# Kernel tuning notes

Hardware: AMD Instinct MI355X
Metric: run time of the kernel (lower is better)

Reference implementation:

```python
import jax, jax.numpy as jnp
import numpy as np

# Architecture constants (match init_kwargs)
L, M, K, P, G = 3, 4096, 2, 4, 4
NUM_IN, NUM_OUT, B = 8192, 1000, 2048
F = 6          # number of combinact activation functions
EPS_BN = 1e-5  # BatchNorm1d eps
EPS = 1e-12    # numeric safety for sqrt


def setup_inputs() -> dict:
    key = jax.random.key(0)
    ks = jax.random.split(key, 8)
    x = jax.random.normal(ks[0], (B, NUM_IN), jnp.float32)
    # shuffle maps: perm 0 is identity (the un-permuted copy), perms 1..P-1 random
    rng = np.random.default_rng(0)
    perms = np.stack([
        np.stack([np.arange(M)] + [rng.permutation(M) for _ in range(P - 1)])
        for _ in range(L)
    ]).astype(np.int32)  # (L, P, M)
    cin_g = NUM_IN // G  # per-group input width (curr stays 8192 every layer)
    W = jax.random.normal(ks[1], (L, G, M // G, cin_g), jnp.float32) / np.sqrt(cin_g)
    b = jax.random.normal(ks[2], (L, G, M // G), jnp.float32) * 0.01
    gamma = jnp.ones((L, M), jnp.float32)
    beta = jnp.zeros((L, M), jnp.float32)
    # original inits alpha_primes to zeros; small random gives non-degenerate mixing
    alpha = jax.random.normal(ks[3], (L, P, F), jnp.float32) * 0.1
    d_last = (M // K) * P
    W_out = jax.random.normal(ks[4], (NUM_OUT, d_last), jnp.float32) / np.sqrt(d_last)
    b_out = jnp.zeros((NUM_OUT,), jnp.float32)
    return {"x": x, "perms": jnp.asarray(perms), "W": W, "b": b,
            "gamma": gamma, "beta": beta, "alpha": alpha,
            "W_out": W_out, "b_out": b_out}


def _combinact(z, alpha_l):
    # z: (B, clusters, K, P) -> (B, clusters, P); per-perm softmax mixing
    sig = jax.nn.sigmoid(z)
    pr = jnp.prod(z, axis=2)
    acts = jnp.stack([
        jnp.max(z, axis=2),                          # max
        jnp.sign(pr) * jnp.sqrt(jnp.abs(pr) + EPS),  # signed geomean (k=2)
        z[:, :, 0, :] * jnp.prod(sig, axis=2),       # swish-k
        jnp.sqrt(jnp.sum(z * z, axis=2) + EPS),      # l2
        jnp.max(jnp.abs(z), axis=2),                 # linf
        jax.nn.logsumexp(z, axis=2),                 # lse
    ], axis=0)  # (F, B, clusters, P)
    w = jax.nn.softmax(alpha_l, axis=-1)  # (P, F)
    return jnp.einsum('fbcp,pf->bcp', acts, w)


def _forward(x, perms, W, b, gamma, beta, alpha, W_out, b_out):
    h = x
    for l in range(L):
        C = h.shape[1]
        # grouped small linears: (B, C/G, G) x (G, M/G, C/G) -> (B, M/G, G) -> (B, M)
        hr = h.reshape(B, C // G, G)
        y = jnp.einsum('bcg,gmc->bmg', hr, W[l]) + b[l].T[None]
        y = y.reshape(B, M)
        # BatchNorm1d (training mode, biased batch var)
        mu = jnp.mean(y, axis=0)
        var = jnp.mean((y - mu) ** 2, axis=0)
        y = (y - mu) * jax.lax.rsqrt(var + EPS_BN) * gamma[l] + beta[l]
        # p permuted copies, reshape into clusters of k
        zc = y[:, perms[l]]                                   # (B, P, M) gather
        z = jnp.transpose(zc, (0, 2, 1)).reshape(B, M // K, K, P)
        a = _combinact(z, alpha[l])                           # (B, M/K, P)
        h = jnp.transpose(a, (0, 2, 1)).reshape(B, (M // K) * P)
    return h @ W_out.T + b_out


def reference(x, perms, W, b, gamma, beta, alpha, W_out, b_out):
    return _forward(x, perms, W, b, gamma, beta, alpha, W_out, b_out)
```

## Files before the change

kernel.cpp:

```cpp
#include <hip/hip_runtime.h>
#include <math.h>

#define Lnum 3
#define Mdim 4096
#define Pdim 4
#define Gdim 4
#define NIN 8192
#define NOUT 1000
#define Bdim 2048
#define Fdim 6
#define CIN 2048
#define MG 1024
#define CH 2048
#define DNEXT 8192
#define NRCHUNK (Bdim / 128)

typedef short bf16x8 __attribute__((ext_vector_type(8)));
typedef float f32x4 __attribute__((ext_vector_type(4)));

__device__ __forceinline__ short f2bf(float f) {
    union { float f; unsigned u; } v; v.f = f;
    unsigned u = v.u;
    unsigned r = (u + 0x7fffu + ((u >> 16) & 1u)) >> 16;
    return (short)r;
}
__device__ __forceinline__ float bf2f(short h) {
    union { unsigned u; float f; } x;
    x.u = ((unsigned)(unsigned short)h) << 16;
    return x.f;
}

__global__ __launch_bounds__(256) void convert_f32_bf16(
    const float* __restrict__ src, short* __restrict__ dst, int n8)
{
    int i = blockIdx.x * 256 + threadIdx.x;
    if (i >= n8) return;
    const float4* s = (const float4*)src + (size_t)i * 2;
    float4 v0 = s[0], v1 = s[1];
    bf16x8 o;
    o[0] = f2bf(v0.x); o[1] = f2bf(v0.y); o[2] = f2bf(v0.z); o[3] = f2bf(v0.w);
    o[4] = f2bf(v1.x); o[5] = f2bf(v1.y); o[6] = f2bf(v1.z); o[7] = f2bf(v1.w);
    *((bf16x8*)dst + i) = o;
}

__global__ __launch_bounds__(256) void convert_wo(
    const float* __restrict__ src, short* __restrict__ dst)
{
    int i = blockIdx.x * 256 + threadIdx.x;
    int row = i >> 10;
    bf16x8 o;
    if (row < NOUT) {
        const float4* s = (const float4*)(src + (size_t)row * DNEXT + (i & 1023) * 8);
        float4 v0 = s[0], v1 = s[1];
        o[0] = f2bf(v0.x); o[1] = f2bf(v0.y); o[2] = f2bf(v0.z); o[3] = f2bf(v0.w);
        o[4] = f2bf(v1.x); o[5] = f2bf(v1.y); o[6] = f2bf(v1.z); o[7] = f2bf(v1.w);
    } else {
        for (int j = 0; j < 8; ++j) o[j] = 0;
    }
    *((bf16x8*)dst + i) = o;
}

__global__ __launch_bounds__(256) void x_to_grouped(
    const float* __restrict__ x, short* __restrict__ hg)
{
    const int c = blockIdx.x * 256 + threadIdx.x;
    const int b = blockIdx.y;
    float4 v = *(const float4*)(x + (size_t)b * NIN + 4 * c);
    const size_t plane = (size_t)Bdim * CIN;
    hg[0 * plane + (size_t)b * CIN + c] = f2bf(v.x);
    hg[1 * plane + (size_t)b * CIN + c] = f2bf(v.y);
    hg[2 * plane + (size_t)b * CIN + c] = f2bf(v.z);
    hg[3 * plane + (size_t)b * CIN + c] = f2bf(v.w);
}

__global__ __launch_bounds__(256) void remap_perms(
    const int* __restrict__ perm, int* __restrict__ perm_g, int n)
{
    int i = blockIdx.x * 256 + threadIdx.x;
    if (i >= n) return;
    int j  = perm[i];
    int jg = ((j & 3) << 10) | (j >> 2);
    perm_g[i] = jg ^ ((jg >> 3) & 3);
}

template<int BN_T, int NWARP, bool STATS, typename CT>
__global__ __launch_bounds__(NWARP * 64) void gemm_mfma(
    const short* __restrict__ A0, size_t aZ, int lda,
    const short* __restrict__ B0, size_t bZ, int ldb,
    const float* __restrict__ bias0, size_t biasZ,
    CT* __restrict__ C0, size_t cZ,
    int K, int ldc, int nbound,
    float* __restrict__ psum, float* __restrict__ psumsq, int sgz)
{
    constexpr int NT   = NWARP * 64;
    constexpr int WCN  = NWARP / 2;
    constexpr int WCOL = BN_T / WCN;
    constexpr int FN   = WCOL / 16;

    const int nx = gridDim.x, ny = gridDim.y;
    const int nwg = nx * ny * gridDim.z;
    const int lin = blockIdx.x + nx * (blockIdx.y + ny * blockIdx.z);
    int swz = (lin & 7) * (nwg >> 3) + (lin >> 3);
    const int bx = swz % nx; swz /= nx;
    const int by = swz % ny;
    const int g  = swz / ny;

    const short* A  = A0 + aZ * g;
    const short* Bm = B0 + bZ * g;
    CT* C = C0 + cZ * g;

    const int n0 = bx * BN_T;
    const int b0 = by * 128;

    __shared__ short As[2][128 * 64];
    __shared__ short Bs[2][BN_T * 64];

    const int tid  = threadIdx.x;
    const int w    = tid >> 6;
    const int lane = tid & 63;
    const int wr = w / WCN, wc = w % WCN;

    f32x4 acc[4][FN];
#pragma unroll
    for (int m = 0; m < 4; ++m)
#pragma unroll
        for (int n = 0; n < FN; ++n) acc[m][n] = (f32x4)0.f;

    auto stage = [&](int buf, int k0) {
#pragma unroll
        for (int idx = tid; idx < 128 * 8; idx += NT) {
            const int r = idx >> 3, slot = idx & 7;
            const int gs = slot ^ (r & 7);
            const short* ga = A + (size_t)(b0 + r) * lda + k0 + gs * 8;
            __builtin_amdgcn_global_load_lds(
                (const __attribute__((address_space(1))) void*)ga,
                (__attribute__((address_space(3))) void*)(&As[buf][idx * 8]), 16, 0, 0);
        }
#pragma unroll
        for (int idx = tid; idx < BN_T * 8; idx += NT) {
            const int r = idx >> 3, slot = idx & 7;
            const int gs = slot ^ (r & 7);
            const short* gb = Bm + (size_t)(n0 + r) * ldb + k0 + gs * 8;
            __builtin_amdgcn_global_load_lds(
                (const __attribute__((address_space(1))) void*)gb,
                (__attribute__((address_space(3))) void*)(&Bs[buf][idx * 8]), 16, 0, 0);
        }
    };

    const int fr15 = lane & 15;
    const int fq   = lane >> 4;

    auto compute = [&](int buf) {
#pragma unroll
        for (int kk = 0; kk < 2; ++kk) {
            bf16x8 af[4], bff[FN];
            const int kob = kk * 64 + fq * 16;
#pragma unroll
            for (int m = 0; m < 4; ++m) {
                const int r  = wr * 64 + m * 16 + fr15;
                const int sw = kob ^ ((r & 7) << 4);
                af[m] = *(const bf16x8*)(&As[buf][r * 64 + (sw >> 1)]);
            }
#pragma unroll
            for (int n = 0; n < FN; ++n) {
                const int r  = wc * WCOL + n * 16 + fr15;
                const int sw = kob ^ ((r & 7) << 4);
                bff[n] = *(const bf16x8*)(&Bs[buf][r * 64 + (sw >> 1)]);
            }
#pragma unroll
            for (int m = 0; m < 4; ++m)
#pragma unroll
                for (int n = 0; n < FN; ++n)
                    acc[m][n] = __builtin_amdgcn_mfma_f32_16x16x32_bf16(af[m], bff[n], acc[m][n], 0, 0, 0);
        }
    };

    stage(0, 0);

    const int nt = K >> 6;
    int p = 0;
    for (int t = 0; t < nt - 1; ++t) {
        stage(p ^ 1, (t + 1) << 6);
        asm volatile("s_waitcnt vmcnt(4)" ::: "memory");
        __builtin_amdgcn_s_barrier();
        asm volatile("" ::: "memory");
        compute(p);
        asm volatile("" ::: "memory");
        __builtin_amdgcn_s_barrier();
        p ^= 1;
    }
    asm volatile("s_waitcnt vmcnt(0)" ::: "memory");
    __builtin_amdgcn_s_barrier();
    asm volatile("" ::: "memory");
    compute(p);

    float s[FN], ss[FN];
#pragma unroll
    for (int n = 0; n < FN; ++n) { s[n] = 0.f; ss[n] = 0.f; }

#pragma unroll
    for (int m = 0; m < 4; ++m) {
#pragma unroll
        for (int n = 0; n < FN; ++n) {
#pragma unroll
            for (int j = 0; j < 4; ++j) {
                const int row = b0 + wr * 64 + m * 16 + fq * 4 + j;
                const int col = n0 + wc * WCOL + n * 16 + fr15;
                if (col < nbound) {
                    float v = acc[m][n][j];
                    if (bias0) v += bias0[biasZ * g + col];
                    C[(size_t)row * ldc + col] = (CT)(sizeof(CT) == 2 ? (CT)f2bf(v) : (CT)v);
                    if (STATS) { s[n] += v; ss[n] += v * v; }
                }
            }
        }
    }

    if (STATS) {
        __syncthreads();
        float* sum_lds = (float*)&As[0][0];
        float* ssq_lds = sum_lds + BN_T * 8;
        const int slot = wr * 4 + fq;
#pragma unroll
        for (int n = 0; n < FN; ++n) {
            const int cl = wc * WCOL + n * 16 + fr15;
            sum_lds[cl * 8 + slot] = s[n];
            ssq_lds[cl * 8 + slot] = ss[n];
        }
        __syncthreads();
        for (int cl = tid; cl < BN_T; cl += NT) {
            float a = 0.f, b = 0.f;
#pragma unroll
            for (int q = 0; q < 8; ++q) {
                a += sum_lds[cl * 8 + q];
                b += ssq_lds[cl * 8 + q];
            }
            const size_t o = (size_t)by * Mdim + g * sgz + n0 + cl;
            psum[o]   = a;
            psumsq[o] = b;
        }
    }
}

__global__ __launch_bounds__(256) void reduce_out(
    const float* __restrict__ part, const float* __restrict__ bo,
    float* __restrict__ out)
{
    const int n = blockIdx.x * 256 + threadIdx.x;
    const int b = blockIdx.y;
    if (n >= NOUT) return;
    const size_t S = (size_t)Bdim * 1024;
    const size_t i = (size_t)b * 1024 + n;
    out[(size_t)b * NOUT + n] =
        part[i] + part[S + i] + part[2 * S + i] + part[3 * S + i] + bo[n];
}

__global__ __launch_bounds__(256) void bn_finalize(
    const float* __restrict__ psum, const float* __restrict__ psumsq,
    const float* __restrict__ gamma, const float* __restrict__ beta,
    float* __restrict__ scale, float* __restrict__ shift)
{
    const int jg = blockIdx.x * 256 + threadIdx.x;
    if (jg >= Mdim) return;
    const int j = ((jg & 1023) << 2) | (jg >> 10);
    float s = 0.f, ss = 0.f;
    for (int r = 0; r < NRCHUNK; ++r) {
        s  += psum[r * Mdim + jg];
        ss += psumsq[r * Mdim + jg];
    }
    const float mu  = s * (1.f / Bdim);
    const float var = ss * (1.f / Bdim) - mu * mu;
    const float sc  = gamma[j] * rsqrtf(var + 1e-5f);
    scale[jg] = sc;
    shift[jg] = beta[j] - mu * sc;
}

__global__ void alpha_softmax(const float* __restrict__ alpha, float* __restrict__ wsm)
{
    const int idx = threadIdx.x;
    if (idx >= Lnum * Pdim) return;
    const float* a = alpha + idx * Fdim;
    float mx = a[0];
#pragma unroll
    for (int f = 1; f < Fdim; ++f) mx = fmaxf(mx, a[f]);
    float e[Fdim]; float s = 0.f;
#pragma unroll
    for (int f = 0; f < Fdim; ++f) { e[f] = __expf(a[f] - mx); s += e[f]; }
    const float inv = 1.f / s;
#pragma unroll
    for (int f = 0; f < Fdim; ++f) wsm[idx * Fdim + f] = e[f] * inv;
}

template<int MODE>
__global__ __launch_bounds__(256) void combinact_kernel(
    const short* __restrict__ Y, const float* __restrict__ scale,
    const float* __restrict__ shift, const int* __restrict__ perm,
    const float* __restrict__ wsm, short* __restrict__ out)
{
    __shared__ f32x4 yn4[Mdim];
    const int b0  = blockIdx.x * 4;
    const int tid = threadIdx.x;

#pragma unroll
    for (int k = 0; k < 2; ++k) {
        const int i8   = k * 256 + tid;
        const int base = i8 * 8;
        const bf16x8 v0 = *((const bf16x8*)(Y + (size_t)(b0 + 0) * Mdim) + i8);
        const bf16x8 v1 = *((const bf16x8*)(Y + (size_t)(b0 + 1) * Mdim) + i8);
        const bf16x8 v2 = *((const bf16x8*)(Y + (size_t)(b0 + 2) * Mdim) + i8);
        const bf16x8 v3 = *((const bf16x8*)(Y + (size_t)(b0 + 3) * Mdim) + i8);
        const int xr = i8 & 3;
#pragma unroll
        for (int jj = 0; jj < 8; ++jj) {
            const float sc = scale[base + jj];
            const float sh = shift[base + jj];
            f32x4 t;
            t[0] = bf2f(v0[jj]) * sc + sh;
            t[1] = bf2f(v1[jj]) * sc + sh;
            t[2] = bf2f(v2[jj]) * sc + sh;
            t[3] = bf2f(v3[jj]) * sc + sh;
            yn4[base + (jj ^ xr)] = t;
        }
    }
    __syncthreads();

    float wv[Pdim][Fdim];
#pragma unroll
    for (int p = 0; p < Pdim; ++p)
#pragma unroll
        for (int f = 0; f < Fdim; ++f) wv[p][f] = wsm[p * Fdim + f];

    const float L2E = 1.44269504f;
    const float LN2 = 0.69314718f;
    const size_t plane = (size_t)Bdim * CIN;

#pragma unroll
    for (int k = 0; k < 8; ++k) {
        const int idx = k * 256 + tid;
        int c, g = 0, q = 0;
        if (MODE == 0) { g = idx >> 9; q = idx & 511; c = q * 4 + g; }
        else           { c = idx; }

#pragma unroll
        for (int p = 0; p < Pdim; ++p) {
            const int2 jj = *(const int2*)(perm + p * Mdim + 2 * c);
            const f32x4 z0v = yn4[jj.x];
            const f32x4 z1v = yn4[jj.y];

#pragma unroll
            for (int r = 0; r < 4; ++r) {
                const float z0 = z0v[r];
                const float z1 = z1v[r];

                const float mx = fmaxf(z0, z1);
                const float pr = z0 * z1;
                const float a1 = copysignf(__builtin_amdgcn_sqrtf(fabsf(pr) + 1e-12f), pr);

                const float e0 = __builtin_amdgcn_exp2f(-L2E * z0);
                const float e1 = __builtin_amdgcn_exp2f(-L2E * z1);
                const float a2 = z0 * __builtin_amdgcn_rcpf((1.f + e0) * (1.f + e1));

                const float a3 = __builtin_amdgcn_sqrtf(z0 * z0 + z1 * z1 + 1e-12f);
                const float a4 = fmaxf(fabsf(z0), fabsf(z1));

                const float ed = __builtin_amdgcn_exp2f(-L2E * fabsf(z0 - z1));
                const float a5 = mx + LN2 * __builtin_amdgcn_logf(1.f + ed);

                const float v = wv[p][0] * mx + wv[p][1] * a1 + wv[p][2] * a2 +
                                wv[p][3] * a3 + wv[p][4] * a4 + wv[p][5] * a5;

                if (MODE == 0)
                    out[g * plane + (size_t)(b0 + r) * CIN + p * 512 + q] = f2bf(v);
                else
                    out[(size_t)(b0 + r) * DNEXT + p * CH + c] = f2bf(v);
            }
        }
    }
}

extern "C" void kernel_launch(void* const* d_in, const int* in_sizes, int n_in,
                              void* d_out, int out_size, void* d_ws, size_t ws_size,
                              hipStream_t stream)
{
    const float* x     = (const float*)d_in[0];
    const int*   perms = (const int*)  d_in[1];
    const float* W     = (const float*)d_in[2];
    const float* bvec  = (const float*)d_in[3];
    const float* gamma = (const float*)d_in[4];
    const float* beta  = (const float*)d_in[5];
    const float* alpha = (const float*)d_in[6];
    const float* Wo    = (const float*)d_in[7];
    const float* bo    = (const float*)d_in[8];
    float* out = (float*)d_out;

    char* ws = (char*)d_ws;
    short* y      = (short*)ws;
    short* hg     = y + (size_t)Bdim * Mdim;
    short* Wlb3   = hg + (size_t)Gdim * Bdim * CIN;
    short* Wob    = Wlb3 + (size_t)Lnum * Gdim * MG * CIN;
    float* psum   = (float*)(Wob + (size_t)1024 * DNEXT);
    float* psumsq = psum + (size_t)NRCHUNK * Mdim;
    float* scale  = psumsq + (size_t)NRCHUNK * Mdim;
    float* shift  = scale + Mdim;
    float* wsm    = shift + Mdim;
    int*   perm_g = (int*)(wsm + Lnum * Pdim * Fdim);

    short* hflat = hg;
    float* part  = (float*)Wlb3;

    alpha_softmax<<<1, 64, 0, stream>>>(alpha, wsm);
    remap_perms<<<(Lnum * Pdim * Mdim) / 256, 256, 0, stream>>>(
        perms, perm_g, Lnum * Pdim * Mdim);
    convert_f32_bf16<<<(Lnum * Gdim * MG * CIN / 8) / 256, 256, 0, stream>>>(
        W, Wlb3, Lnum * Gdim * MG * CIN / 8);
    convert_wo<<<(1024 * 1024) / 256, 256, 0, stream>>>(Wo, Wob);
    x_to_grouped<<<dim3(CIN / 256, Bdim), 256, 0, stream>>>(x, hg);

    const size_t planeA = (size_t)Bdim * CIN;
    const size_t planeB = (size_t)MG * CIN;

    for (int l = 0; l < Lnum; ++l) {
        dim3 gg(MG / 128, Bdim / 128, Gdim);
        gemm_mfma<128, 8, true, short><<<gg, 512, 0, stream>>>(
            hg, planeA, CIN, Wlb3 + (size_t)l * Gdim * MG * CIN, planeB, CIN,
            bvec + (size_t)l * Gdim * MG, (size_t)MG,
            y, (size_t)MG,
            CIN, Mdim, MG,
            psum, psumsq, MG);

        bn_finalize<<<Mdim / 256, 256, 0, stream>>>(
            psum, psumsq, gamma + (size_t)l * Mdim, beta + (size_t)l * Mdim, scale, shift);

        if (l < Lnum - 1)
            combinact_kernel<0><<<Bdim / 4, 256, 0, stream>>>(
                y, scale, shift, perm_g + (size_t)l * Pdim * Mdim, wsm + l * Pdim * Fdim, hg);
        else
            combinact_kernel<1><<<Bdim / 4, 256, 0, stream>>>(
                y, scale, shift, perm_g + (size_t)l * Pdim * Mdim, wsm + l * Pdim * Fdim, hflat);
    }

    dim3 go(1024 / 128, Bdim / 128, 4);
    gemm_mfma<128, 8, false, float><<<go, 512, 0, stream>>>(
        hflat, (size_t)2048, DNEXT, Wob, (size_t)2048, DNEXT,
        nullptr, 0,
        part, (size_t)Bdim * 1024,
        2048, 1024, 1024,
        nullptr, nullptr, 0);

    dim3 gr(4, Bdim);
    reduce_out<<<gr, 256, 0, stream>>>(part, bo, out);
}
```

Before: 316.2 us.

## Fuse weight fp32-to-bf16 conversion into GEMM B staging and precompute exps in combinact

Removes the separate weight conversion kernels. The GEMMs now read fp32 weights directly, convert them in registers and write the swizzled bf16 into LDS, with the pipeline restructured so the global loads overlap compute. The combinact kernel now handles 2 batch rows per block and stores exp(z) alongside z in shared memory. It then derives swish, and logsumexp as log(E0+E1), from the stored exps instead of recomputing three exps per pair. The GEMMs read twice the weight bytes and convert them repeatedly across tiles, and log(E0+E1) can overflow for large z.

```diff
diff --git a/kernel.cpp b/kernel.cpp
--- a/kernel.cpp
+++ b/kernel.cpp
@@ -1,4 +1,5 @@
 #include <hip/hip_runtime.h>
+#include <hip/hip_bf16.h>
 #include <math.h>
 
 #define Lnum 3
@@ -30,36 +31,6 @@
     return x.f;
 }
 
-__global__ __launch_bounds__(256) void convert_f32_bf16(
-    const float* __restrict__ src, short* __restrict__ dst, int n8)
-{
-    int i = blockIdx.x * 256 + threadIdx.x;
-    if (i >= n8) return;
-    const float4* s = (const float4*)src + (size_t)i * 2;
-    float4 v0 = s[0], v1 = s[1];
-    bf16x8 o;
-    o[0] = f2bf(v0.x); o[1] = f2bf(v0.y); o[2] = f2bf(v0.z); o[3] = f2bf(v0.w);
-    o[4] = f2bf(v1.x); o[5] = f2bf(v1.y); o[6] = f2bf(v1.z); o[7] = f2bf(v1.w);
-    *((bf16x8*)dst + i) = o;
-}
-
-__global__ __launch_bounds__(256) void convert_wo(
-    const float* __restrict__ src, short* __restrict__ dst)
-{
-    int i = blockIdx.x * 256 + threadIdx.x;
-    int row = i >> 10;
-    bf16x8 o;
-    if (row < NOUT) {
-        const float4* s = (const float4*)(src + (size_t)row * DNEXT + (i & 1023) * 8);
-        float4 v0 = s[0], v1 = s[1];
-        o[0] = f2bf(v0.x); o[1] = f2bf(v0.y); o[2] = f2bf(v0.z); o[3] = f2bf(v0.w);
-        o[4] = f2bf(v1.x); o[5] = f2bf(v1.y); o[6] = f2bf(v1.z); o[7] = f2bf(v1.w);
-    } else {
-        for (int j = 0; j < 8; ++j) o[j] = 0;
-    }
-    *((bf16x8*)dst + i) = o;
-}
-
 __global__ __launch_bounds__(256) void x_to_grouped(
     const float* __restrict__ x, short* __restrict__ hg)
 {
@@ -86,7 +57,7 @@
 template<int BN_T, int NWARP, bool STATS, typename CT>
 __global__ __launch_bounds__(NWARP * 64) void gemm_mfma(
     const short* __restrict__ A0, size_t aZ, int lda,
-    const short* __restrict__ B0, size_t bZ, int ldb,
+    const float* __restrict__ B0, size_t bZ, int ldb, int bclamp,
     const float* __restrict__ bias0, size_t biasZ,
     CT* __restrict__ C0, size_t cZ,
     int K, int ldc, int nbound,
@@ -106,7 +77,7 @@
     const int g  = swz / ny;
 
     const short* A  = A0 + aZ * g;
-    const short* Bm = B0 + bZ * g;
+    const float* Bf = B0 + bZ * g;
     CT* C = C0 + cZ * g;
 
     const int n0 = bx * BN_T;
@@ -126,7 +97,7 @@
 #pragma unroll
         for (int n = 0; n < FN; ++n) acc[m][n] = (f32x4)0.f;
 
-    auto stage = [&](int buf, int k0) {
+    auto stageA = [&](int buf, int k0) {
 #pragma unroll
         for (int idx = tid; idx < 128 * 8; idx += NT) {
             const int r = idx >> 3, slot = idx & 7;
@@ -136,15 +107,30 @@
                 (const __attribute__((address_space(1))) void*)ga,
                 (__attribute__((address_space(3))) void*)(&As[buf][idx * 8]), 16, 0, 0);
         }
-#pragma unroll
-        for (int idx = tid; idx < BN_T * 8; idx += NT) {
-            const int r = idx >> 3, slot = idx & 7;
-            const int gs = slot ^ (r & 7);
-            const short* gb = Bm + (size_t)(n0 + r) * ldb + k0 + gs * 8;
-            __builtin_amdgcn_global_load_lds(
-                (const __attribute__((address_space(1))) void*)gb,
-                (__attribute__((address_space(3))) void*)(&Bs[buf][idx * 8]), 16, 0, 0);
-        }
+    };
+
+    static_assert(NT == BN_T * 4, "B-staging mapping assumes 4 threads/row");
+    const int brow = tid >> 2;
+    const int bq   = tid & 3;
+    float4 br0, br1, br2, br3;
+    auto issueB = [&](int k0) {
+        const int rr = min(n0 + brow, bclamp - 1);
+        const float* p = Bf + (size_t)rr * ldb + k0 + bq * 16;
+        br0 = *(const float4*)(p);
+        br1 = *(const float4*)(p + 4);
+        br2 = *(const float4*)(p + 8);
+        br3 = *(const float4*)(p + 12);
+    };
+    auto writeB = [&](int buf) {
+        bf16x8 o0, o1;
+        o0[0] = f2bf(br0.x); o0[1] = f2bf(br0.y); o0[2] = f2bf(br0.z); o0[3] = f2bf(br0.w);
+        o0[4] = f2bf(br1.x); o0[5] = f2bf(br1.y); o0[6] = f2bf(br1.z); o0[7] = f2bf(br1.w);
+        o1[0] = f2bf(br2.x); o1[1] = f2bf(br2.y); o1[2] = f2bf(br2.z); o1[3] = f2bf(br2.w);
+        o1[4] = f2bf(br3.x); o1[5] = f2bf(br3.y); o1[6] = f2bf(br3.z); o1[7] = f2bf(br3.w);
+        const int s0 = (2 * bq)     ^ (brow & 7);
+        const int s1 = (2 * bq + 1) ^ (brow & 7);
+        *(bf16x8*)(&Bs[buf][brow * 64 + s0 * 8]) = o0;
+        *(bf16x8*)(&Bs[buf][brow * 64 + s1 * 8]) = o1;
     };
 
     const int fr15 = lane & 15;
@@ -175,24 +161,28 @@
         }
     };
 
-    stage(0, 0);
+    stageA(0, 0);
+    issueB(0);
+    asm volatile("s_waitcnt vmcnt(0)" ::: "memory");
+    writeB(0);
+    asm volatile("s_waitcnt lgkmcnt(0)" ::: "memory");
+    __builtin_amdgcn_s_barrier();
+    asm volatile("" ::: "memory");
 
     const int nt = K >> 6;
     int p = 0;
-    for (int t = 0; t < nt - 1; ++t) {
-        stage(p ^ 1, (t + 1) << 6);
-        asm volatile("s_waitcnt vmcnt(4)" ::: "memory");
+    for (int t = 0; t < nt; ++t) {
+        if (t + 1 < nt) { stageA(p ^ 1, (t + 1) << 6); issueB((t + 1) << 6); }
+        compute(p);
+        if (t + 1 < nt) {
+            asm volatile("s_waitcnt vmcnt(0)" ::: "memory");
+            writeB(p ^ 1);
+        }
+        asm volatile("s_waitcnt lgkmcnt(0)" ::: "memory");
         __builtin_amdgcn_s_barrier();
         asm volatile("" ::: "memory");
-        compute(p);
-        asm volatile("" ::: "memory");
-        __builtin_amdgcn_s_barrier();
         p ^= 1;
     }
-    asm volatile("s_waitcnt vmcnt(0)" ::: "memory");
-    __builtin_amdgcn_s_barrier();
-    asm volatile("" ::: "memory");
-    compute(p);
 
     float s[FN], ss[FN];
 #pragma unroll
@@ -297,9 +287,11 @@
     const float* __restrict__ shift, const int* __restrict__ perm,
     const float* __restrict__ wsm, short* __restrict__ out)
 {
-    __shared__ f32x4 yn4[Mdim];
-    const int b0  = blockIdx.x * 4;
+    __shared__ f32x4 zE[Mdim];
+    const int b0  = blockIdx.x * 2;
     const int tid = threadIdx.x;
+    const float L2E = 1.44269504f;
+    const float LN2 = 0.69314718f;
 
 #pragma unroll
     for (int k = 0; k < 2; ++k) {
@@ -307,8 +299,6 @@
         const int base = i8 * 8;
         const bf16x8 v0 = *((const bf16x8*)(Y + (size_t)(b0 + 0) * Mdim) + i8);
         const bf16x8 v1 = *((const bf16x8*)(Y + (size_t)(b0 + 1) * Mdim) + i8);
-        const bf16x8 v2 = *((const bf16x8*)(Y + (size_t)(b0 + 2) * Mdim) + i8);
-        const bf16x8 v3 = *((const bf16x8*)(Y + (size_t)(b0 + 3) * Mdim) + i8);
         const int xr = i8 & 3;
 #pragma unroll
         for (int jj = 0; jj < 8; ++jj) {
@@ -317,9 +307,9 @@
             f32x4 t;
             t[0] = bf2f(v0[jj]) * sc + sh;
             t[1] = bf2f(v1[jj]) * sc + sh;
-            t[2] = bf2f(v2[jj]) * sc + sh;
-            t[3] = bf2f(v3[jj]) * sc + sh;
-            yn4[base + (jj ^ xr)] = t;
+            t[2] = __builtin_amdgcn_exp2f(L2E * t[0]);
+            t[3] = __builtin_amdgcn_exp2f(L2E * t[1]);
+            zE[base + (jj ^ xr)] = t;
         }
     }
     __syncthreads();
@@ -330,8 +320,6 @@
 #pragma unroll
         for (int f = 0; f < Fdim; ++f) wv[p][f] = wsm[p * Fdim + f];
 
-    const float L2E = 1.44269504f;
-    const float LN2 = 0.69314718f;
     const size_t plane = (size_t)Bdim * CIN;
 
 #pragma unroll
@@ -344,27 +332,22 @@
 #pragma unroll
         for (int p = 0; p < Pdim; ++p) {
             const int2 jj = *(const int2*)(perm + p * Mdim + 2 * c);
-            const f32x4 z0v = yn4[jj.x];
-            const f32x4 z1v = yn4[jj.y];
-
-#pragma unroll
-            for (int r = 0; r < 4; ++r) {
-                const float z0 = z0v[r];
-                const float z1 = z1v[r];
+            const f32x4 c0 = zE[jj.x];
+            const f32x4 c1 = zE[jj.y];
+
+#pragma unroll
+            for (int r = 0; r < 2; ++r) {
+                const float z0 = c0[r],     z1 = c1[r];
+                const float E0 = c0[2 + r], E1 = c1[2 + r];
 
                 const float mx = fmaxf(z0, z1);
                 const float pr = z0 * z1;
                 const float a1 = copysignf(__builtin_amdgcn_sqrtf(fabsf(pr) + 1e-12f), pr);
-
-                const float e0 = __builtin_amdgcn_exp2f(-L2E * z0);
-                const float e1 = __builtin_amdgcn_exp2f(-L2E * z1);
-                const float a2 = z0 * __builtin_amdgcn_rcpf((1.f + e0) * (1.f + e1));
-
+                const float a2 = z0 * E0 * E1 *
+                                 __builtin_amdgcn_rcpf((1.f + E0) * (1.f + E1));
                 const float a3 = __builtin_amdgcn_sqrtf(z0 * z0 + z1 * z1 + 1e-12f);
                 const float a4 = fmaxf(fabsf(z0), fabsf(z1));
-
-                const float ed = __builtin_amdgcn_exp2f(-L2E * fabsf(z0 - z1));
-                const float a5 = mx + LN2 * __builtin_amdgcn_logf(1.f + ed);
+                const float a5 = LN2 * __builtin_amdgcn_logf(E0 + E1);
 
                 const float v = wv[p][0] * mx + wv[p][1] * a1 + wv[p][2] * a2 +
                                 wv[p][3] * a3 + wv[p][4] * a4 + wv[p][5] * a5;
@@ -396,9 +379,8 @@
     char* ws = (char*)d_ws;
     short* y      = (short*)ws;
     short* hg     = y + (size_t)Bdim * Mdim;
-    short* Wlb3   = hg + (size_t)Gdim * Bdim * CIN;
-    short* Wob    = Wlb3 + (size_t)Lnum * Gdim * MG * CIN;
-    float* psum   = (float*)(Wob + (size_t)1024 * DNEXT);
+    float* part   = (float*)(hg + (size_t)Gdim * Bdim * CIN);
+    float* psum   = part + (size_t)4 * Bdim * 1024;
     float* psumsq = psum + (size_t)NRCHUNK * Mdim;
     float* scale  = psumsq + (size_t)NRCHUNK * Mdim;
     float* shift  = scale + Mdim;
@@ -406,14 +388,10 @@
     int*   perm_g = (int*)(wsm + Lnum * Pdim * Fdim);
 
     short* hflat = hg;
-    float* part  = (float*)Wlb3;
 
     alpha_softmax<<<1, 64, 0, stream>>>(alpha, wsm);
     remap_perms<<<(Lnum * Pdim * Mdim) / 256, 256, 0, stream>>>(
         perms, perm_g, Lnum * Pdim * Mdim);
-    convert_f32_bf16<<<(Lnum * Gdim * MG * CIN / 8) / 256, 256, 0, stream>>>(
-        W, Wlb3, Lnum * Gdim * MG * CIN / 8);
-    convert_wo<<<(1024 * 1024) / 256, 256, 0, stream>>>(Wo, Wob);
     x_to_grouped<<<dim3(CIN / 256, Bdim), 256, 0, stream>>>(x, hg);
 
     const size_t planeA = (size_t)Bdim * CIN;
@@ -422,7 +400,8 @@
     for (int l = 0; l < Lnum; ++l) {
         dim3 gg(MG / 128, Bdim / 128, Gdim);
         gemm_mfma<128, 8, true, short><<<gg, 512, 0, stream>>>(
-            hg, planeA, CIN, Wlb3 + (size_t)l * Gdim * MG * CIN, planeB, CIN,
+            hg, planeA, CIN,
+            W + (size_t)l * Gdim * MG * CIN, planeB, CIN, MG,
             bvec + (size_t)l * Gdim * MG, (size_t)MG,
             y, (size_t)MG,
             CIN, Mdim, MG,
@@ -432,16 +411,17 @@
             psum, psumsq, gamma + (size_t)l * Mdim, beta + (size_t)l * Mdim, scale, shift);
 
         if (l < Lnum - 1)
-            combinact_kernel<0><<<Bdim / 4, 256, 0, stream>>>(
+            combinact_kernel<0><<<Bdim / 2, 256, 0, stream>>>(
                 y, scale, shift, perm_g + (size_t)l * Pdim * Mdim, wsm + l * Pdim * Fdim, hg);
         else
-            combinact_kernel<1><<<Bdim / 4, 256, 0, stream>>>(
+            combinact_kernel<1><<<Bdim / 2, 256, 0, stream>>>(
                 y, scale, shift, perm_g + (size_t)l * Pdim * Mdim, wsm + l * Pdim * Fdim, hflat);
     }
 
     dim3 go(1024 / 128, Bdim / 128, 4);
     gemm_mfma<128, 8, false, float><<<go, 512, 0, stream>>>(
-        hflat, (size_t)2048, DNEXT, Wob, (size_t)2048, DNEXT,
+        hflat, (size_t)2048, DNEXT,
+        Wo, (size_t)2048, DNEXT, NOUT,
         nullptr, 0,
         part, (size_t)Bdim * 1024,
         2048, 1024, 1024,
```

After: 367.2 us. 16.1% more time.
